# Kernel optimization log

Hardware: AMD Instinct MI355X
Metric: run time of the kernel (lower is better)

The kernel has to match this reference:

```python
import jax, jax.numpy as jnp
import numpy as np

GH, GW = 8, 8  # hypernetwork patch grid
EPS = 1e-5


def image_coords(b, h, w, dtype):
    # matches get_image_coordinates: channel0 = x (varies along W), channel1 = y (varies along H)
    xs = jnp.linspace(-1.0, 1.0, w, dtype=dtype)
    ys = jnp.linspace(-1.0, 1.0, h, dtype=dtype)
    X = jnp.broadcast_to(xs[None, :], (h, w))
    Y = jnp.broadcast_to(ys[:, None], (h, w))
    g = jnp.stack([X, Y], axis=0)  # [2,H,W]
    return jnp.broadcast_to(g[None], (b, 2, h, w))


def im2col3(x):
    # reflect-pad 3x3 im2col -> [B,C,9,H,W]
    H, W = x.shape[2], x.shape[3]
    xp = jnp.pad(x, ((0, 0), (0, 0), (1, 1), (1, 1)), mode='reflect')
    cols = [xp[:, :, i:i + H, j:j + W] for i in range(3) for j in range(3)]
    return jnp.stack(cols, axis=2)


def meta_dw3(x, wsig):
    # depthwise 3x3 conv with per-patch weights. wsig: [B, C*9, GH, GW]
    B, C, H, W = x.shape
    p, q = H // GH, W // GW
    cols = im2col3(x).reshape(B, C, 9, GH, p, GW, q)
    Wd = wsig.reshape(B, C, 9, GH, GW)
    out = jnp.einsum('bctuivj,bctuv->bcuivj', cols, Wd)
    return out.reshape(B, C, H, W)


def meta_pw(x, wsig, out_nc):
    # pointwise 1x1 conv with per-patch weights. wsig: [B, out_nc*C, GH, GW]
    B, C, H, W = x.shape
    p, q = H // GH, W // GW
    xr = x.reshape(B, C, GH, p, GW, q)
    Wp = wsig.reshape(B, out_nc, C, GH, GW)
    out = jnp.einsum('bcuivj,bocuv->bouivj', xr, Wp)
    return out.reshape(B, out_nc, H, W)


def batch_norm(x, g, b):
    m = jnp.mean(x, (0, 2, 3), keepdims=True)
    v = jnp.var(x, (0, 2, 3), keepdims=True)
    return (x - m) * jax.lax.rsqrt(v + EPS) * g[None, :, None, None] + b[None, :, None, None]


def relu6(x):
    return jnp.clip(x, 0.0, 6.0)


def hpir(x, wsig, out_nc, g_dw, b_dw, g_pw, b_pw):
    # HyperPatchInvertedResidual, expand_ratio=1, stride=1, in_nc != out_nc -> no residual
    C = x.shape[1]
    n_dw = C * 9
    h = relu6(batch_norm(meta_dw3(x, wsig[:, :n_dw]), g_dw, b_dw))
    h = batch_norm(meta_pw(h, wsig[:, n_dw:n_dw + out_nc * C], out_nc), g_pw, b_pw)
    return h


def resize_bilinear(p, hw):
    B, C = p.shape[0], p.shape[1]
    return jax.image.resize(p, (B, C, hw[0], hw[1]), method='bilinear')


def decoder_forward(x_img, f0, f1, w0, w1, w2,
                    g_dw0, b_dw0, g_pw0, b_pw0,
                    g_dw1, b_dw1, g_pw1, b_pw1,
                    g_dw2, b_dw2, g_pw2, b_pw2):
    feats = [x_img, f0, f1]  # [img] + features[:-1]
    level_w = [w0, w1, w2]
    level_out = [64, 32, 21]
    bn_p = [(g_dw0, b_dw0, g_pw0, b_pw0),
            (g_dw1, b_dw1, g_pw1, b_pw1),
            (g_dw2, b_dw2, g_pw2, b_pw2)]
    p = None
    for level in range(3):
        f = feats[-level - 1]
        if p is None:
            p = f
        else:
            if p.shape[2:] != f.shape[2:]:
                p = resize_bilinear(p, f.shape[2:])
            p = jnp.concatenate([f, p], axis=1)
        B, _, H, W = p.shape
        p = jnp.concatenate([image_coords(B, H, W, p.dtype), p], axis=1)
        g_dw, b_dw, g_pw, b_pw = bn_p[level]
        p = hpir(p, level_w[level], level_out[level], g_dw, b_dw, g_pw, b_pw)
    return p


def setup_inputs() -> dict:
    key = jax.random.key(0)
    ks = jax.random.split(key, 8)
    inp = {
        'x_img': jax.random.normal(ks[0], (4, 3, 256, 256), jnp.float32),
        'f0': jax.random.normal(ks[1], (4, 32, 64, 64), jnp.float32),
        'f1': jax.random.normal(ks[2], (4, 64, 32, 32), jnp.float32),
        'w0': jax.random.normal(ks[3], (4, 4818, 8, 8), jnp.float32) * 0.1,
        'w1': jax.random.normal(ks[4], (4, 4018, 8, 8), jnp.float32) * 0.1,
        'w2': jax.random.normal(ks[5], (4, 1110, 8, 8), jnp.float32) * 0.1,
    }
    for name, c in [('dw0', 66), ('pw0', 64), ('dw1', 98), ('pw1', 32), ('dw2', 37), ('pw2', 21)]:
        inp['g_' + name] = jnp.ones((c,), jnp.float32)
        inp['b_' + name] = jnp.zeros((c,), jnp.float32)
    return inp


def reference(x_img, f0, f1, w0, w1, w2,
              g_dw0, b_dw0, g_pw0, b_pw0,
              g_dw1, b_dw1, g_pw1, b_pw1,
              g_dw2, b_dw2, g_pw2, b_pw2):
    return decoder_forward(x_img, f0, f1, w0, w1, w2,
                           g_dw0, b_dw0, g_pw0, b_pw0,
                           g_dw1, b_dw1, g_pw1, b_pw1,
                           g_dw2, b_dw2, g_pw2, b_pw2)
```

## Files before the change

### kernel.cpp

```cpp
#include <hip/hip_runtime.h>
#include <hip/hip_bf16.h>

#define EPS 1e-5f

__device__ __forceinline__ int reflect_idx(int i, int n) {
    if (i < 0) return -i;
    if (i >= n) return 2 * n - 2 - i;
    return i;
}

__device__ __forceinline__ float bilin(const float* __restrict__ pb, int Hp, float sy, float sx) {
    int y0 = (int)floorf(sy), x0 = (int)floorf(sx);
    float fy = sy - y0, fx = sx - x0;
    int y0c = min(max(y0, 0), Hp - 1), y1c = min(max(y0 + 1, 0), Hp - 1);
    int x0c = min(max(x0, 0), Hp - 1), x1c = min(max(x0 + 1, 0), Hp - 1);
    float v00 = pb[y0c * Hp + x0c], v01 = pb[y0c * Hp + x1c];
    float v10 = pb[y1c * Hp + x0c], v11 = pb[y1c * Hp + x1c];
    return v00 * (1 - fy) * (1 - fx) + v01 * (1 - fy) * fx
         + v10 * fy * (1 - fx) + v11 * fy * fx;
}

template <int LEVEL, bool WRITE>
__global__ __launch_bounds__(256)
void fused_dw_kernel(const float* __restrict__ feat, const float* __restrict__ prev,
                     const float* __restrict__ pss, const float* __restrict__ wsig,
                     float* __restrict__ out, float* __restrict__ part) {
    constexpr int C    = LEVEL == 0 ? 66 : 98;
    constexpr int H    = LEVEL == 0 ? 32 : 64;
    constexpr int TILE = 16;
    constexpr int NT   = H / TILE;
    constexpr int PXPT = (TILE * TILE) / 256;
    constexpr int WC   = LEVEL == 0 ? 4818 : 4018;
    constexpr int NF   = LEVEL == 0 ? 64 : 32;
    constexpr int Hp   = 32;
    constexpr int Cp   = 64;
    constexpr int P    = H / 8;
    constexpr float SC = 0.5f;
    constexpr int HS   = TILE + 2;

    __shared__ float sh[HS * HS];
    int tid = threadIdx.x, bid = blockIdx.x;
    int tile = bid % (NT * NT);
    int c = (bid / (NT * NT)) % C;
    int b = bid / (NT * NT * C);
    int ty0 = (tile / NT) * TILE, tx0 = (tile % NT) * TILE;

    for (int i = tid; i < HS * HS; i += 256) {
        int h = reflect_idx(ty0 - 1 + i / HS, H);
        int w = reflect_idx(tx0 - 1 + i % HS, H);
        float val;
        if (c == 0)      val = -1.f + 2.f * w / (H - 1);
        else if (c == 1) val = -1.f + 2.f * h / (H - 1);
        else if (c < 2 + NF) val = feat[((size_t)(b * NF + c - 2) * H + h) * H + w];
        else {
            int o = c - 2 - NF;
            const float* pb = prev + (size_t)(b * Cp + o) * Hp * Hp;
            float raw = bilin(pb, Hp, (h + 0.5f) * SC - 0.5f, (w + 0.5f) * SC - 0.5f);
            val = raw * pss[2 * o] + pss[2 * o + 1];
        }
        sh[i] = val;
    }
    __syncthreads();

    float s1 = 0.f, s2 = 0.f;
    float* ob = out + (((size_t)(b * C + c)) * H + ty0) * H + tx0;
    float wreg[9];
    if constexpr (TILE == P) {
        const float* wb = wsig + ((size_t)(b * WC + c * 9)) * 64 + (ty0 / P) * 8 + (tx0 / P);
#pragma unroll
        for (int t = 0; t < 9; ++t) wreg[t] = wb[(size_t)t * 64];
    }
#pragma unroll
    for (int k = 0; k < PXPT; ++k) {
        int px = tid + k * 256;
        int tyy = px / TILE, txx = px % TILE;
        if constexpr (TILE != P) {
            int u = (ty0 + tyy) / P, vv = (tx0 + txx) / P;
            const float* wb = wsig + ((size_t)(b * WC + c * 9)) * 64 + u * 8 + vv;
#pragma unroll
            for (int t = 0; t < 9; ++t) wreg[t] = wb[(size_t)t * 64];
        }
        float acc = 0.f;
#pragma unroll
        for (int t = 0; t < 9; ++t)
            acc += wreg[t] * sh[(tyy + t / 3) * HS + txx + t % 3];
        if constexpr (WRITE) ob[tyy * H + txx] = acc;
        s1 += acc; s2 += acc * acc;
    }
#pragma unroll
    for (int off = 32; off; off >>= 1) {
        s1 += __shfl_xor(s1, off);
        s2 += __shfl_xor(s2, off);
    }
    __shared__ float r1[4], r2[4];
    int wave = tid >> 6;
    if ((tid & 63) == 0) { r1[wave] = s1; r2[wave] = s2; }
    __syncthreads();
    if (tid == 0) {
        int slot = bid & 63;
        atomicAdd(&part[slot * 2 * C + 2 * c],     r1[0] + r1[1] + r1[2] + r1[3]);
        atomicAdd(&part[slot * 2 * C + 2 * c + 1], r2[0] + r2[1] + r2[2] + r2[3]);
    }
}

__global__ void red_kernel(const float* __restrict__ part, const float* __restrict__ g,
                           const float* __restrict__ bb, float* __restrict__ ss,
                           int C, float invN) {
    int c = threadIdx.x;
    if (c >= C) return;
    float s1 = 0.f, s2 = 0.f;
#pragma unroll 8
    for (int s = 0; s < 64; ++s) {
        s1 += part[s * 2 * C + 2 * c];
        s2 += part[s * 2 * C + 2 * c + 1];
    }
    float m = s1 * invN;
    float var = s2 * invN - m * m;
    float sc = g[c] * rsqrtf(var + EPS);
    ss[2 * c] = sc;
    ss[2 * c + 1] = bb[c] - m * sc;
}

__global__ __launch_bounds__(256)
void dw2_col_kernel(const float* __restrict__ ximg, const float* __restrict__ prev,
                    const float* __restrict__ pw1ss, const float* __restrict__ wsig,
                    __hip_bfloat16* __restrict__ out, float* __restrict__ part) {
    const int C = 37, H = 256, W = 256, WC = 1110, Hp = 64, Cp = 32;
    const int S = 260;
    __shared__ float sh[10 * S];
    __shared__ float pssl[64];
    __shared__ float lwv[72];
    __shared__ float r1[4], r2[4];

    int tid = threadIdx.x, bid = blockIdx.x;
    int rb = bid & 31;
    int c  = (bid >> 5) % C;
    int b  = bid / (32 * C);
    int ty0 = rb * 8;
    int u = rb >> 2;

    if (tid < 64) pssl[tid] = pw1ss[tid];
    if (tid < 72) {
        int v = tid / 9, t = tid - v * 9;
        lwv[tid] = wsig[((size_t)(b * WC + c * 9 + t)) * 64 + u * 8 + v];
    }
    __syncthreads();

    const float* pb   = (c >= 5) ? prev + (size_t)(b * Cp + (c - 5)) * Hp * Hp : nullptr;
    const float* xrow = (c >= 2 && c < 5) ? ximg + (size_t)(b * 3 + c - 2) * H * W : nullptr;
    float cx = -1.f + tid * (2.f / 255.f);
    float sxm = (tid + 0.5f) * 0.25f - 0.5f;
    int x0m = (int)floorf(sxm);
    float fxm = sxm - x0m;
    int x0cm = min(max(x0m, 0), Hp - 1), x1cm = min(max(x0m + 1, 0), Hp - 1);
    float psc = (c >= 5) ? pssl[2 * (c - 5)] : 0.f;
    float psh = (c >= 5) ? pssl[2 * (c - 5) + 1] : 0.f;

    if (c >= 5 && rb >= 1 && rb <= 30) {
        int y0b = 2 * rb - 1;
        const float* q0 = pb + (size_t)y0b * Hp;
        const float* q1 = q0 + Hp;
        const float* q2 = q1 + Hp;
        const float* q3 = q2 + Hp;
        float a0 = q0[x0cm] + (q0[x1cm] - q0[x0cm]) * fxm;
        float a1 = q1[x0cm] + (q1[x1cm] - q1[x0cm]) * fxm;
        float a2 = q2[x0cm] + (q2[x1cm] - q2[x0cm]) * fxm;
        float a3 = q3[x0cm] + (q3[x1cm] - q3[x0cm]) * fxm;
        sh[0 * S + tid + 1] = (a0 + (a1 - a0) * 0.375f) * psc + psh;
        sh[1 * S + tid + 1] = (a0 + (a1 - a0) * 0.625f) * psc + psh;
        sh[2 * S + tid + 1] = (a0 + (a1 - a0) * 0.875f) * psc + psh;
        sh[3 * S + tid + 1] = (a1 + (a2 - a1) * 0.125f) * psc + psh;
        sh[4 * S + tid + 1] = (a1 + (a2 - a1) * 0.375f) * psc + psh;
        sh[5 * S + tid + 1] = (a1 + (a2 - a1) * 0.625f) * psc + psh;
        sh[6 * S + tid + 1] = (a1 + (a2 - a1) * 0.875f) * psc + psh;
        sh[7 * S + tid + 1] = (a2 + (a3 - a2) * 0.125f) * psc + psh;
        sh[8 * S + tid + 1] = (a2 + (a3 - a2) * 0.375f) * psc + psh;
        sh[9 * S + tid + 1] = (a2 + (a3 - a2) * 0.625f) * psc + psh;
    } else {
#pragma unroll
        for (int r = 0; r < 10; ++r) {
            int h = reflect_idx(ty0 - 1 + r, H);
            float val;
            if (c == 0)      val = cx;
            else if (c == 1) val = -1.f + h * (2.f / 255.f);
            else if (c < 5)  val = xrow[h * W + tid];
            else {
                float sy = (h + 0.5f) * 0.25f - 0.5f;
                int y0 = (int)floorf(sy);
                float fy = sy - y0;
                int y0c = min(max(y0, 0), Hp - 1), y1c = min(max(y0 + 1, 0), Hp - 1);
                const float* q0 = pb + y0c * Hp;
                const float* q1 = pb + y1c * Hp;
                float a0 = q0[x0cm] + (q0[x1cm] - q0[x0cm]) * fxm;
                float a1 = q1[x0cm] + (q1[x1cm] - q1[x0cm]) * fxm;
                val = (a0 + (a1 - a0) * fy) * psc + psh;
            }
            sh[r * S + tid + 1] = val;
        }
    }
    if (tid < 20) {
        int r = tid >> 1, side = tid & 1;
        int wimg = side ? 254 : 1;
        int h = reflect_idx(ty0 - 1 + r, H);
        float val;
        if (c == 0)      val = -1.f + wimg * (2.f / 255.f);
        else if (c == 1) val = -1.f + h * (2.f / 255.f);
        else if (c < 5)  val = xrow[h * W + wimg];
        else {
            float sx = (wimg + 0.5f) * 0.25f - 0.5f;
            int x0 = (int)floorf(sx); float fx = sx - x0;
            int x0c = min(max(x0, 0), Hp - 1), x1c = min(max(x0 + 1, 0), Hp - 1);
            float sy = (h + 0.5f) * 0.25f - 0.5f;
            int y0 = (int)floorf(sy); float fy = sy - y0;
            int y0c = min(max(y0, 0), Hp - 1), y1c = min(max(y0 + 1, 0), Hp - 1);
            const float* q0 = pb + y0c * Hp;
            const float* q1 = pb + y1c * Hp;
            float a0 = q0[x0c] + (q0[x1c] - q0[x0c]) * fx;
            float a1 = q1[x0c] + (q1[x1c] - q1[x0c]) * fx;
            val = (a0 + (a1 - a0) * fy) * psc + psh;
        }
        sh[r * S + (side ? 257 : 0)] = val;
    }
    __syncthreads();

    int t = tid;
    int v = t >> 5;
    float wr[9];
#pragma unroll
    for (int tap = 0; tap < 9; ++tap) wr[tap] = lwv[v * 9 + tap];

    float px[8];
#pragma unroll
    for (int k = 0; k < 8; ++k) px[k] = 0.f;

#pragma unroll
    for (int r = 0; r < 10; ++r) {
        float L = sh[r * S + t];
        float M = sh[r * S + t + 1];
        float R = sh[r * S + t + 2];
#pragma unroll
        for (int dr = 0; dr < 3; ++dr) {
            int k = r - dr;
            if (k >= 0 && k < 8)
                px[k] += wr[dr * 3] * L + wr[dr * 3 + 1] * M + wr[dr * 3 + 2] * R;
        }
    }

    __hip_bfloat16* ob = out + (((size_t)(b * C + c)) * H + ty0) * W + t;
    float s1 = 0.f, s2 = 0.f;
#pragma unroll
    for (int k = 0; k < 8; ++k) {
        ob[k * W] = __float2bfloat16(px[k]);
        s1 += px[k]; s2 += px[k] * px[k];
    }
#pragma unroll
    for (int off = 32; off; off >>= 1) {
        s1 += __shfl_xor(s1, off);
        s2 += __shfl_xor(s2, off);
    }
    int wave = tid >> 6;
    if ((tid & 63) == 0) { r1[wave] = s1; r2[wave] = s2; }
    __syncthreads();
    if (tid == 0) {
        int slot = bid & 63;
        atomicAdd(&part[slot * 2 * C + 2 * c],     r1[0] + r1[1] + r1[2] + r1[3]);
        atomicAdd(&part[slot * 2 * C + 2 * c + 1], r2[0] + r2[1] + r2[2] + r2[3]);
    }
}

template <int C, int ONC, int H, int PX_T, int OC_T>
__global__ __launch_bounds__(256)
void pw_small_kernel(const float* __restrict__ x, const float* __restrict__ wsig,
                     const float* __restrict__ ss, float* __restrict__ out,
                     float* __restrict__ part, int WC, int ndw) {
    constexpr int P = H / 8;
    constexpr int OC_I = ONC / OC_T;
    __shared__ float lw[ONC * C];
    __shared__ float lx[C * PX_T];
    int tid = threadIdx.x, bid = blockIdx.x;
    int uv = bid & 63, b = bid >> 6;
    int u = uv >> 3, v = uv & 7;

    const size_t wbase = ((size_t)b * WC + ndw) * 64 + uv;
    for (int i = tid; i < ONC * C; i += 256) lw[i] = wsig[wbase + (size_t)i * 64];
    for (int i = tid; i < C * PX_T; i += 256) {
        int c = i / PX_T, pxl = i % PX_T;
        int h = u * P + pxl / P, w = v * P + pxl % P;
        float xv = x[(((size_t)b * C + c) * H + h) * H + w];
        lx[i] = fminf(fmaxf(xv * ss[2 * c] + ss[2 * c + 1], 0.f), 6.f);
    }
    __syncthreads();

    int px_id = tid % PX_T, oc_id = tid / PX_T;
    int h = u * P + px_id / P, w = v * P + px_id % P;
    float acc[OC_I];
#pragma unroll
    for (int oi = 0; oi < OC_I; ++oi) acc[oi] = 0.f;
    for (int c = 0; c < C; ++c) {
        float xv = lx[c * PX_T + px_id];
#pragma unroll
        for (int oi = 0; oi < OC_I; ++oi)
            acc[oi] += lw[(oc_id * OC_I + oi) * C + c] * xv;
    }
    float* ob = out + (((size_t)b * ONC) * H + h) * H + w;
#pragma unroll
    for (int oi = 0; oi < OC_I; ++oi)
        ob[(size_t)(oc_id * OC_I + oi) * H * H] = acc[oi];

    constexpr int GROUP = (PX_T < 64) ? PX_T : 64;
    int lane = tid & 63;
    int slot = bid & 63;
#pragma unroll
    for (int oi = 0; oi < OC_I; ++oi) {
        float s1 = acc[oi], s2 = acc[oi] * acc[oi];
#pragma unroll
        for (int off = GROUP / 2; off; off >>= 1) {
            s1 += __shfl_xor(s1, off);
            s2 += __shfl_xor(s2, off);
        }
        if ((lane & (GROUP - 1)) == 0) {
            int o = oc_id * OC_I + oi;
            atomicAdd(&part[slot * 2 * ONC + 2 * o], s1);
            atomicAdd(&part[slot * 2 * ONC + 2 * o + 1], s2);
        }
    }
}

__global__ __launch_bounds__(256)
void pw2_kernel(const __hip_bfloat16* __restrict__ x, const float* __restrict__ wsig,
                const float* __restrict__ dss,
                float* __restrict__ out, float* __restrict__ part) {
    const int C = 37, ONC = 21, H = 256, WC = 1110, NDW = 333;
    __shared__ float lw[777];
    __shared__ float ssl[74];
    __shared__ float r1[4][ONC], r2[4][ONC];
    int tid = threadIdx.x, bid = blockIdx.x;
    int chunk = bid & 3;
    int uv = (bid >> 2) & 63;
    int b = bid >> 8;
    int y0 = (uv >> 3) * 32 + chunk * 8, x0 = (uv & 7) * 32;

    for (int i = tid; i < 777; i += 256) lw[i] = wsig[((size_t)(b * WC + NDW) + i) * 64 + uv];
    if (tid < 74) ssl[tid] = dss[tid];
    __syncthreads();

    int row = tid >> 5, col = tid & 31;
    const __hip_bfloat16* xb = x + (((size_t)(b * C)) * H + y0 + row) * H + x0 + col;
    float acc[ONC];
#pragma unroll
    for (int o = 0; o < ONC; ++o) acc[o] = 0.f;

    for (int c = 0; c < C; ++c) {
        float xv = __bfloat162float(xb[(size_t)c * H * H]);
        xv = fminf(fmaxf(xv * ssl[2 * c] + ssl[2 * c + 1], 0.f), 6.f);
#pragma unroll
        for (int o = 0; o < ONC; ++o)
            acc[o] += lw[o * C + c] * xv;
    }
    float* ob = out + (((size_t)(b * ONC)) * H + y0 + row) * H + x0 + col;
#pragma unroll
    for (int o = 0; o < ONC; ++o) ob[(size_t)o * H * H] = acc[o];

    int wave = tid >> 6, lane = tid & 63;
#pragma unroll
    for (int o = 0; o < ONC; ++o) {
        float s1 = acc[o], s2 = acc[o] * acc[o];
#pragma unroll
        for (int off = 32; off; off >>= 1) {
            s1 += __shfl_xor(s1, off);
            s2 += __shfl_xor(s2, off);
        }
        if (lane == 0) { r1[wave][o] = s1; r2[wave][o] = s2; }
    }
    __syncthreads();
    int slot = bid & 63;
    for (int o = tid; o < ONC; o += 256) {
        atomicAdd(&part[slot * 42 + 2 * o],     r1[0][o] + r1[1][o] + r1[2][o] + r1[3][o]);
        atomicAdd(&part[slot * 42 + 2 * o + 1], r2[0][o] + r2[1][o] + r2[2][o] + r2[3][o]);
    }
}

__global__ void finalbn_kernel(float* __restrict__ out, const float* __restrict__ ss) {
    int idx = blockIdx.x * 256 + threadIdx.x;
    const int total4 = 4 * 21 * 256 * 256 / 4;
    if (idx >= total4) return;
    int c = (idx / (256 * 256 / 4)) % 21;
    float4 v = ((float4*)out)[idx];
    float sc = ss[2 * c], sb = ss[2 * c + 1];
    v.x = v.x * sc + sb; v.y = v.y * sc + sb; v.z = v.z * sc + sb; v.w = v.w * sc + sb;
    ((float4*)out)[idx] = v;
}

extern "C" void kernel_launch(void* const* d_in, const int* in_sizes, int n_in,
                              void* d_out, int out_size, void* d_ws, size_t ws_size,
                              hipStream_t stream) {
    const float* x_img = (const float*)d_in[0];
    const float* f0    = (const float*)d_in[1];
    const float* f1    = (const float*)d_in[2];
    const float* w0    = (const float*)d_in[3];
    const float* w1    = (const float*)d_in[4];
    const float* w2    = (const float*)d_in[5];
    const float* g_dw0 = (const float*)d_in[6],  *b_dw0 = (const float*)d_in[7];
    const float* g_pw0 = (const float*)d_in[8],  *b_pw0 = (const float*)d_in[9];
    const float* g_dw1 = (const float*)d_in[10], *b_dw1 = (const float*)d_in[11];
    const float* g_pw1 = (const float*)d_in[12], *b_pw1 = (const float*)d_in[13];
    const float* g_dw2 = (const float*)d_in[14], *b_dw2 = (const float*)d_in[15];
    const float* g_pw2 = (const float*)d_in[16], *b_pw2 = (const float*)d_in[17];
    float* out = (float*)d_out;
    float* ws = (float*)d_ws;

    float* part_dw0 = ws;
    float* part_pw0 = ws + 8448;
    float* part_dw1 = ws + 16640;
    float* part_pw1 = ws + 29184;
    float* part_dw2 = ws + 33280;
    float* part_pw2 = ws + 38016;
    float* dw0ss = ws + 40704;
    float* pw0ss = ws + 40836;
    float* dw1ss = ws + 40964;
    float* pw1ss = ws + 41160;
    float* dw2ss = ws + 41224;
    float* pw2ss = ws + 41298;
    float* pw0raw = ws + 41344;
    float* pw1raw = pw0raw + 262144;
    float* bigA   = pw1raw + 524288;
    __hip_bfloat16* bigAb = (__hip_bfloat16*)bigA;

    hipMemsetAsync(ws, 0, 40704 * sizeof(float), stream);

    fused_dw_kernel<0, true><<<4 * 66 * 4, 256, 0, stream>>>(
        f1, nullptr, nullptr, w0, bigA, part_dw0);
    red_kernel<<<1, 128, 0, stream>>>(part_dw0, g_dw0, b_dw0, dw0ss, 66, 1.f / 4096.f);
    pw_small_kernel<66, 64, 32, 16, 16><<<256, 256, 0, stream>>>(
        bigA, w0, dw0ss, pw0raw, part_pw0, 4818, 594);
    red_kernel<<<1, 128, 0, stream>>>(part_pw0, g_pw0, b_pw0, pw0ss, 64, 1.f / 4096.f);
    fused_dw_kernel<1, true><<<4 * 98 * 16, 256, 0, stream>>>(
        f0, pw0raw, pw0ss, w1, bigA, part_dw1);
    red_kernel<<<1, 128, 0, stream>>>(part_dw1, g_dw1, b_dw1, dw1ss, 98, 1.f / 16384.f);
    pw_small_kernel<98, 32, 64, 64, 4><<<256, 256, 0, stream>>>(
        bigA, w1, dw1ss, pw1raw, part_pw1, 4018, 882);
    red_kernel<<<1, 128, 0, stream>>>(part_pw1, g_pw1, b_pw1, pw1ss, 32, 1.f / 16384.f);
    dw2_col_kernel<<<4 * 37 * 32, 256, 0, stream>>>(
        x_img, pw1raw, pw1ss, w2, bigAb, part_dw2);
    red_kernel<<<1, 128, 0, stream>>>(part_dw2, g_dw2, b_dw2, dw2ss, 37, 1.f / 262144.f);
    pw2_kernel<<<1024, 256, 0, stream>>>(bigAb, w2, dw2ss, out, part_pw2);
    red_kernel<<<1, 128, 0, stream>>>(part_pw2, g_pw2, b_pw2, pw2ss, 21, 1.f / 262144.f);
    finalbn_kernel<<<5376, 256, 0, stream>>>(out, pw2ss);
}
```

Baseline: 144.0 us.

## Fuse all decoder stages into one persistent cooperative kernel with grid syncs

```diff
diff --git a/kernel.cpp b/kernel.cpp
--- a/kernel.cpp
+++ b/kernel.cpp
@@ -1,5 +1,8 @@
 #include <hip/hip_runtime.h>
 #include <hip/hip_bf16.h>
+#include <hip/hip_cooperative_groups.h>
+
+namespace cg = cooperative_groups;
 
 #define EPS 1e-5f
 
@@ -20,11 +23,31 @@
          + v10 * fy * (1 - fx) + v11 * fy * fx;
 }
 
-template <int LEVEL, bool WRITE>
-__global__ __launch_bounds__(256)
-void fused_dw_kernel(const float* __restrict__ feat, const float* __restrict__ prev,
-                     const float* __restrict__ pss, const float* __restrict__ wsig,
-                     float* __restrict__ out, float* __restrict__ part) {
+__device__ __forceinline__ void block_red(const float* __restrict__ part,
+                                          const float* __restrict__ g,
+                                          const float* __restrict__ bb,
+                                          float* ssl, int C, float invN, int tid) {
+    if (tid < C) {
+        float s1 = 0.f, s2 = 0.f;
+#pragma unroll 8
+        for (int s = 0; s < 64; ++s) {
+            s1 += part[s * 2 * C + 2 * tid];
+            s2 += part[s * 2 * C + 2 * tid + 1];
+        }
+        float m = s1 * invN;
+        float var = s2 * invN - m * m;
+        float sc = g[tid] * rsqrtf(var + EPS);
+        ssl[2 * tid] = sc;
+        ssl[2 * tid + 1] = bb[tid] - m * sc;
+    }
+}
+
+template <int LEVEL>
+__device__ __forceinline__
+void dw_body(int bid, int tid, float* BODY,
+             const float* __restrict__ feat, const float* __restrict__ prev,
+             const float* __restrict__ pssl, const float* __restrict__ wsig,
+             float* __restrict__ out, float* __restrict__ part) {
     constexpr int C    = LEVEL == 0 ? 66 : 98;
     constexpr int H    = LEVEL == 0 ? 32 : 64;
     constexpr int TILE = 16;
@@ -38,8 +61,10 @@
     constexpr float SC = 0.5f;
     constexpr int HS   = TILE + 2;
 
-    __shared__ float sh[HS * HS];
-    int tid = threadIdx.x, bid = blockIdx.x;
+    float* sh = BODY;
+    float* r1 = BODY + 324;
+    float* r2 = BODY + 328;
+
     int tile = bid % (NT * NT);
     int c = (bid / (NT * NT)) % C;
     int b = bid / (NT * NT * C);
@@ -56,7 +81,7 @@
             int o = c - 2 - NF;
             const float* pb = prev + (size_t)(b * Cp + o) * Hp * Hp;
             float raw = bilin(pb, Hp, (h + 0.5f) * SC - 0.5f, (w + 0.5f) * SC - 0.5f);
-            val = raw * pss[2 * o] + pss[2 * o + 1];
+            val = raw * pssl[2 * o] + pssl[2 * o + 1];
         }
         sh[i] = val;
     }
@@ -65,16 +90,11 @@
     float s1 = 0.f, s2 = 0.f;
     float* ob = out + (((size_t)(b * C + c)) * H + ty0) * H + tx0;
     float wreg[9];
-    if constexpr (TILE == P) {
-        const float* wb = wsig + ((size_t)(b * WC + c * 9)) * 64 + (ty0 / P) * 8 + (tx0 / P);
-#pragma unroll
-        for (int t = 0; t < 9; ++t) wreg[t] = wb[(size_t)t * 64];
-    }
 #pragma unroll
     for (int k = 0; k < PXPT; ++k) {
         int px = tid + k * 256;
         int tyy = px / TILE, txx = px % TILE;
-        if constexpr (TILE != P) {
+        {
             int u = (ty0 + tyy) / P, vv = (tx0 + txx) / P;
             const float* wb = wsig + ((size_t)(b * WC + c * 9)) * 64 + u * 8 + vv;
 #pragma unroll
@@ -84,7 +104,7 @@
 #pragma unroll
         for (int t = 0; t < 9; ++t)
             acc += wreg[t] * sh[(tyy + t / 3) * HS + txx + t % 3];
-        if constexpr (WRITE) ob[tyy * H + txx] = acc;
+        ob[tyy * H + txx] = acc;
         s1 += acc; s2 += acc * acc;
     }
 #pragma unroll
@@ -92,7 +112,6 @@
         s1 += __shfl_xor(s1, off);
         s2 += __shfl_xor(s2, off);
     }
-    __shared__ float r1[4], r2[4];
     int wave = tid >> 6;
     if ((tid & 63) == 0) { r1[wave] = s1; r2[wave] = s2; }
     __syncthreads();
@@ -103,43 +122,85 @@
     }
 }
 
-__global__ void red_kernel(const float* __restrict__ part, const float* __restrict__ g,
-                           const float* __restrict__ bb, float* __restrict__ ss,
-                           int C, float invN) {
-    int c = threadIdx.x;
-    if (c >= C) return;
-    float s1 = 0.f, s2 = 0.f;
-#pragma unroll 8
-    for (int s = 0; s < 64; ++s) {
-        s1 += part[s * 2 * C + 2 * c];
-        s2 += part[s * 2 * C + 2 * c + 1];
-    }
-    float m = s1 * invN;
-    float var = s2 * invN - m * m;
-    float sc = g[c] * rsqrtf(var + EPS);
-    ss[2 * c] = sc;
-    ss[2 * c + 1] = bb[c] - m * sc;
-}
-
-__global__ __launch_bounds__(256)
-void dw2_col_kernel(const float* __restrict__ ximg, const float* __restrict__ prev,
-                    const float* __restrict__ pw1ss, const float* __restrict__ wsig,
-                    __hip_bfloat16* __restrict__ out, float* __restrict__ part) {
+template <int C, int ONC, int H, int PX_T, int OC_T>
+__device__ __forceinline__
+void pw_small_body(int bid, int tid, float* BODY,
+                   const float* __restrict__ x, const float* __restrict__ wsig,
+                   const float* __restrict__ ssl, float* __restrict__ out,
+                   float* __restrict__ part, int WC, int ndw) {
+    constexpr int P = H / 8;
+    constexpr int OC_I = ONC / OC_T;
+    float* lw = BODY;
+    float* lx = BODY + ONC * C;
+
+    __syncthreads();
+
+    int uv = bid & 63, b = bid >> 6;
+    int u = uv >> 3, v = uv & 7;
+
+    const size_t wbase = ((size_t)b * WC + ndw) * 64 + uv;
+    for (int i = tid; i < ONC * C; i += 256) lw[i] = wsig[wbase + (size_t)i * 64];
+    for (int i = tid; i < C * PX_T; i += 256) {
+        int c = i / PX_T, pxl = i % PX_T;
+        int h = u * P + pxl / P, w = v * P + pxl % P;
+        float xv = x[(((size_t)b * C + c) * H + h) * H + w];
+        lx[i] = fminf(fmaxf(xv * ssl[2 * c] + ssl[2 * c + 1], 0.f), 6.f);
+    }
+    __syncthreads();
+
+    int px_id = tid % PX_T, oc_id = tid / PX_T;
+    int h = u * P + px_id / P, w = v * P + px_id % P;
+    float acc[OC_I];
+#pragma unroll
+    for (int oi = 0; oi < OC_I; ++oi) acc[oi] = 0.f;
+    for (int c = 0; c < C; ++c) {
+        float xv = lx[c * PX_T + px_id];
+#pragma unroll
+        for (int oi = 0; oi < OC_I; ++oi)
+            acc[oi] += lw[(oc_id * OC_I + oi) * C + c] * xv;
+    }
+    float* ob = out + (((size_t)b * ONC) * H + h) * H + w;
+#pragma unroll
+    for (int oi = 0; oi < OC_I; ++oi)
+        ob[(size_t)(oc_id * OC_I + oi) * H * H] = acc[oi];
+
+    constexpr int GROUP = (PX_T < 64) ? PX_T : 64;
+    int lane = tid & 63;
+    int slot = bid & 63;
+#pragma unroll
+    for (int oi = 0; oi < OC_I; ++oi) {
+        float s1 = acc[oi], s2 = acc[oi] * acc[oi];
+#pragma unroll
+        for (int off = GROUP / 2; off; off >>= 1) {
+            s1 += __shfl_xor(s1, off);
+            s2 += __shfl_xor(s2, off);
+        }
+        if ((lane & (GROUP - 1)) == 0) {
+            int o = oc_id * OC_I + oi;
+            atomicAdd(&part[slot * 2 * ONC + 2 * o], s1);
+            atomicAdd(&part[slot * 2 * ONC + 2 * o + 1], s2);
+        }
+    }
+}
+
+__device__ __forceinline__
+void dw2_body(int bid, int tid, float* BODY,
+              const float* __restrict__ ximg, const float* __restrict__ prev,
+              const float* __restrict__ pssl, const float* __restrict__ wsig,
+              __hip_bfloat16* __restrict__ out, float* __restrict__ part) {
     const int C = 37, H = 256, W = 256, WC = 1110, Hp = 64, Cp = 32;
     const int S = 260;
-    __shared__ float sh[10 * S];
-    __shared__ float pssl[64];
-    __shared__ float lwv[72];
-    __shared__ float r1[4], r2[4];
-
-    int tid = threadIdx.x, bid = blockIdx.x;
+    float* sh  = BODY;
+    float* lwv = BODY + 2600;
+    float* r1  = BODY + 2672;
+    float* r2  = BODY + 2676;
+
     int rb = bid & 31;
     int c  = (bid >> 5) % C;
     int b  = bid / (32 * C);
     int ty0 = rb * 8;
     int u = rb >> 2;
 
-    if (tid < 64) pssl[tid] = pw1ss[tid];
     if (tid < 72) {
         int v = tid / 9, t = tid - v * 9;
         lwv[tid] = wsig[((size_t)(b * WC + c * 9 + t)) * 64 + u * 8 + v];
@@ -263,85 +324,29 @@
     __syncthreads();
     if (tid == 0) {
         int slot = bid & 63;
-        atomicAdd(&part[slot * 2 * C + 2 * c],     r1[0] + r1[1] + r1[2] + r1[3]);
+        atomicAdd(&part[slot * 2 * C + 2 * c],     s1 * 0.f + r1[0] + r1[1] + r1[2] + r1[3]);
         atomicAdd(&part[slot * 2 * C + 2 * c + 1], r2[0] + r2[1] + r2[2] + r2[3]);
     }
 }
 
-template <int C, int ONC, int H, int PX_T, int OC_T>
-__global__ __launch_bounds__(256)
-void pw_small_kernel(const float* __restrict__ x, const float* __restrict__ wsig,
-                     const float* __restrict__ ss, float* __restrict__ out,
-                     float* __restrict__ part, int WC, int ndw) {
-    constexpr int P = H / 8;
-    constexpr int OC_I = ONC / OC_T;
-    __shared__ float lw[ONC * C];
-    __shared__ float lx[C * PX_T];
-    int tid = threadIdx.x, bid = blockIdx.x;
-    int uv = bid & 63, b = bid >> 6;
-    int u = uv >> 3, v = uv & 7;
-
-    const size_t wbase = ((size_t)b * WC + ndw) * 64 + uv;
-    for (int i = tid; i < ONC * C; i += 256) lw[i] = wsig[wbase + (size_t)i * 64];
-    for (int i = tid; i < C * PX_T; i += 256) {
-        int c = i / PX_T, pxl = i % PX_T;
-        int h = u * P + pxl / P, w = v * P + pxl % P;
-        float xv = x[(((size_t)b * C + c) * H + h) * H + w];
-        lx[i] = fminf(fmaxf(xv * ss[2 * c] + ss[2 * c + 1], 0.f), 6.f);
-    }
-    __syncthreads();
-
-    int px_id = tid % PX_T, oc_id = tid / PX_T;
-    int h = u * P + px_id / P, w = v * P + px_id % P;
-    float acc[OC_I];
-#pragma unroll
-    for (int oi = 0; oi < OC_I; ++oi) acc[oi] = 0.f;
-    for (int c = 0; c < C; ++c) {
-        float xv = lx[c * PX_T + px_id];
-#pragma unroll
-        for (int oi = 0; oi < OC_I; ++oi)
-            acc[oi] += lw[(oc_id * OC_I + oi) * C + c] * xv;
-    }
-    float* ob = out + (((size_t)b * ONC) * H + h) * H + w;
-#pragma unroll
-    for (int oi = 0; oi < OC_I; ++oi)
-        ob[(size_t)(oc_id * OC_I + oi) * H * H] = acc[oi];
-
-    constexpr int GROUP = (PX_T < 64) ? PX_T : 64;
-    int lane = tid & 63;
-    int slot = bid & 63;
-#pragma unroll
-    for (int oi = 0; oi < OC_I; ++oi) {
-        float s1 = acc[oi], s2 = acc[oi] * acc[oi];
-#pragma unroll
-        for (int off = GROUP / 2; off; off >>= 1) {
-            s1 += __shfl_xor(s1, off);
-            s2 += __shfl_xor(s2, off);
-        }
-        if ((lane & (GROUP - 1)) == 0) {
-            int o = oc_id * OC_I + oi;
-            atomicAdd(&part[slot * 2 * ONC + 2 * o], s1);
-            atomicAdd(&part[slot * 2 * ONC + 2 * o + 1], s2);
-        }
-    }
-}
-
-__global__ __launch_bounds__(256)
-void pw2_kernel(const __hip_bfloat16* __restrict__ x, const float* __restrict__ wsig,
-                const float* __restrict__ dss,
-                float* __restrict__ out, float* __restrict__ part) {
+__device__ __forceinline__
+void pw2_body(int bid, int tid, float* BODY,
+              const __hip_bfloat16* __restrict__ x, const float* __restrict__ wsig,
+              const float* __restrict__ ssl, float* __restrict__ out,
+              float* __restrict__ part) {
     const int C = 37, ONC = 21, H = 256, WC = 1110, NDW = 333;
-    __shared__ float lw[777];
-    __shared__ float ssl[74];
-    __shared__ float r1[4][ONC], r2[4][ONC];
-    int tid = threadIdx.x, bid = blockIdx.x;
+    float* lw = BODY;
+    float (*r1)[ONC] = (float(*)[ONC])(BODY + 784);
+    float (*r2)[ONC] = (float(*)[ONC])(BODY + 872);
+
+    __syncthreads();
+
     int chunk = bid & 3;
     int uv = (bid >> 2) & 63;
     int b = bid >> 8;
     int y0 = (uv >> 3) * 32 + chunk * 8, x0 = (uv & 7) * 32;
 
     for (int i = tid; i < 777; i += 256) lw[i] = wsig[((size_t)(b * WC + NDW) + i) * 64 + uv];
-    if (tid < 74) ssl[tid] = dss[tid];
     __syncthreads();
 
     int row = tid >> 5, col = tid & 31;
@@ -380,70 +385,114 @@
     }
 }
 
-__global__ void finalbn_kernel(float* __restrict__ out, const float* __restrict__ ss) {
-    int idx = blockIdx.x * 256 + threadIdx.x;
+struct MegaArgs {
+    const float *x_img, *f0, *f1, *w0, *w1, *w2;
+    const float *g_dw0, *b_dw0, *g_pw0, *b_pw0;
+    const float *g_dw1, *b_dw1, *g_pw1, *b_pw1;
+    const float *g_dw2, *b_dw2, *g_pw2, *b_pw2;
+    float* out;
+    float* parts;
+    float* part_dw0; float* part_pw0; float* part_dw1;
+    float* part_pw1; float* part_dw2; float* part_pw2;
+    float* pw0raw; float* pw1raw; float* bigA;
+    __hip_bfloat16* bigAb;
+};
+
+__global__ __launch_bounds__(256, 4)
+void mega_kernel(MegaArgs a) {
+    cg::grid_group grid = cg::this_grid();
+    __shared__ float smem[9664];
+    float* SSL  = smem;
+    float* BODY = smem + 256;
+    int tid = threadIdx.x, bx = blockIdx.x, nb = gridDim.x;
+
+    for (int i = bx * 256 + tid; i < 40704; i += nb * 256) a.parts[i] = 0.f;
+    grid.sync();
+
+    for (int vb = bx; vb < 1056; vb += nb)
+        dw_body<0>(vb, tid, BODY, a.f1, nullptr, nullptr, a.w0, a.bigA, a.part_dw0);
+    grid.sync();
+
+    block_red(a.part_dw0, a.g_dw0, a.b_dw0, SSL, 66, 1.f / 4096.f, tid);
+    for (int vb = bx; vb < 256; vb += nb)
+        pw_small_body<66, 64, 32, 16, 16>(vb, tid, BODY, a.bigA, a.w0, SSL, a.pw0raw,
+                                          a.part_pw0, 4818, 594);
+    grid.sync();
+
+    block_red(a.part_pw0, a.g_pw0, a.b_pw0, SSL, 64, 1.f / 4096.f, tid);
+    __syncthreads();
+    for (int vb = bx; vb < 6272; vb += nb)
+        dw_body<1>(vb, tid, BODY, a.f0, a.pw0raw, SSL, a.w1, a.bigA, a.part_dw1);
+    grid.sync();
+
+    block_red(a.part_dw1, a.g_dw1, a.b_dw1, SSL, 98, 1.f / 16384.f, tid);
+    for (int vb = bx; vb < 256; vb += nb)
+        pw_small_body<98, 32, 64, 64, 4>(vb, tid, BODY, a.bigA, a.w1, SSL, a.pw1raw,
+                                         a.part_pw1, 4018, 882);
+    grid.sync();
+
+    block_red(a.part_pw1, a.g_pw1, a.b_pw1, SSL, 32, 1.f / 16384.f, tid);
+    __syncthreads();
+    for (int vb = bx; vb < 4736; vb += nb)
+        dw2_body(vb, tid, BODY, a.x_img, a.pw1raw, SSL, a.w2, a.bigAb, a.part_dw2);
+    grid.sync();
+
+    block_red(a.part_dw2, a.g_dw2, a.b_dw2, SSL, 37, 1.f / 262144.f, tid);
+    for (int vb = bx; vb < 1024; vb += nb)
+        pw2_body(vb, tid, BODY, a.bigAb, a.w2, SSL, a.out, a.part_pw2);
+    grid.sync();
+
+    block_red(a.part_pw2, a.g_pw2, a.b_pw2, SSL, 21, 1.f / 262144.f, tid);
+    __syncthreads();
     const int total4 = 4 * 21 * 256 * 256 / 4;
-    if (idx >= total4) return;
-    int c = (idx / (256 * 256 / 4)) % 21;
-    float4 v = ((float4*)out)[idx];
-    float sc = ss[2 * c], sb = ss[2 * c + 1];
-    v.x = v.x * sc + sb; v.y = v.y * sc + sb; v.z = v.z * sc + sb; v.w = v.w * sc + sb;
-    ((float4*)out)[idx] = v;
+    for (int idx = bx * 256 + tid; idx < total4; idx += nb * 256) {
+        int c = (idx / (256 * 256 / 4)) % 21;
+        float4 v = ((float4*)a.out)[idx];
+        float sc = SSL[2 * c], sb = SSL[2 * c + 1];
+        v.x = v.x * sc + sb; v.y = v.y * sc + sb; v.z = v.z * sc + sb; v.w = v.w * sc + sb;
+        ((float4*)a.out)[idx] = v;
+    }
 }
 
 extern "C" void kernel_launch(void* const* d_in, const int* in_sizes, int n_in,
                               void* d_out, int out_size, void* d_ws, size_t ws_size,
                               hipStream_t stream) {
-    const float* x_img = (const float*)d_in[0];
-    const float* f0    = (const float*)d_in[1];
-    const float* f1    = (const float*)d_in[2];
-    const float* w0    = (const float*)d_in[3];
-    const float* w1    = (const float*)d_in[4];
-    const float* w2    = (const float*)d_in[5];
-    const float* g_dw0 = (const float*)d_in[6],  *b_dw0 = (const float*)d_in[7];
-    const float* g_pw0 = (const float*)d_in[8],  *b_pw0 = (const float*)d_in[9];
-    const float* g_dw1 = (const float*)d_in[10], *b_dw1 = (const float*)d_in[11];
-    const float* g_pw1 = (const float*)d_in[12], *b_pw1 = (const float*)d_in[13];
-    const float* g_dw2 = (const float*)d_in[14], *b_dw2 = (const float*)d_in[15];
-    const float* g_pw2 = (const float*)d_in[16], *b_pw2 = (const float*)d_in[17];
-    float* out = (float*)d_out;
     float* ws = (float*)d_ws;
 
-    float* part_dw0 = ws;
-    float* part_pw0 = ws + 8448;
-    float* part_dw1 = ws + 16640;
-    float* part_pw1 = ws + 29184;
-    float* part_dw2 = ws + 33280;
-    float* part_pw2 = ws + 38016;
-    float* dw0ss = ws + 40704;
-    float* pw0ss = ws + 40836;
-    float* dw1ss = ws + 40964;
-    float* pw1ss = ws + 41160;
-    float* dw2ss = ws + 41224;
-    float* pw2ss = ws + 41298;
-    float* pw0raw = ws + 41344;
-    float* pw1raw = pw0raw + 262144;
-    float* bigA   = pw1raw + 524288;
-    __hip_bfloat16* bigAb = (__hip_bfloat16*)bigA;
-
-    hipMemsetAsync(ws, 0, 40704 * sizeof(float), stream);
-
-    fused_dw_kernel<0, true><<<4 * 66 * 4, 256, 0, stream>>>(
-        f1, nullptr, nullptr, w0, bigA, part_dw0);
-    red_kernel<<<1, 128, 0, stream>>>(part_dw0, g_dw0, b_dw0, dw0ss, 66, 1.f / 4096.f);
-    pw_small_kernel<66, 64, 32, 16, 16><<<256, 256, 0, stream>>>(
-        bigA, w0, dw0ss, pw0raw, part_pw0, 4818, 594);
-    red_kernel<<<1, 128, 0, stream>>>(part_pw0, g_pw0, b_pw0, pw0ss, 64, 1.f / 4096.f);
-    fused_dw_kernel<1, true><<<4 * 98 * 16, 256, 0, stream>>>(
-        f0, pw0raw, pw0ss, w1, bigA, part_dw1);
-    red_kernel<<<1, 128, 0, stream>>>(part_dw1, g_dw1, b_dw1, dw1ss, 98, 1.f / 16384.f);
-    pw_small_kernel<98, 32, 64, 64, 4><<<256, 256, 0, stream>>>(
-        bigA, w1, dw1ss, pw1raw, part_pw1, 4018, 882);
-    red_kernel<<<1, 128, 0, stream>>>(part_pw1, g_pw1, b_pw1, pw1ss, 32, 1.f / 16384.f);
-    dw2_col_kernel<<<4 * 37 * 32, 256, 0, stream>>>(
-        x_img, pw1raw, pw1ss, w2, bigAb, part_dw2);
-    red_kernel<<<1, 128, 0, stream>>>(part_dw2, g_dw2, b_dw2, dw2ss, 37, 1.f / 262144.f);
-    pw2_kernel<<<1024, 256, 0, stream>>>(bigAb, w2, dw2ss, out, part_pw2);
-    red_kernel<<<1, 128, 0, stream>>>(part_pw2, g_pw2, b_pw2, pw2ss, 21, 1.f / 262144.f);
-    finalbn_kernel<<<5376, 256, 0, stream>>>(out, pw2ss);
-}
+    MegaArgs a;
+    a.x_img = (const float*)d_in[0];
+    a.f0    = (const float*)d_in[1];
+    a.f1    = (const float*)d_in[2];
+    a.w0    = (const float*)d_in[3];
+    a.w1    = (const float*)d_in[4];
+    a.w2    = (const float*)d_in[5];
+    a.g_dw0 = (const float*)d_in[6];  a.b_dw0 = (const float*)d_in[7];
+    a.g_pw0 = (const float*)d_in[8];  a.b_pw0 = (const float*)d_in[9];
+    a.g_dw1 = (const float*)d_in[10]; a.b_dw1 = (const float*)d_in[11];
+    a.g_pw1 = (const float*)d_in[12]; a.b_pw1 = (const float*)d_in[13];
+    a.g_dw2 = (const float*)d_in[14]; a.b_dw2 = (const float*)d_in[15];
+    a.g_pw2 = (const float*)d_in[16]; a.b_pw2 = (const float*)d_in[17];
+    a.out   = (float*)d_out;
+
+    a.parts    = ws;
+    a.part_dw0 = ws;
+    a.part_pw0 = ws + 8448;
+    a.part_dw1 = ws + 16640;
+    a.part_pw1 = ws + 29184;
+    a.part_dw2 = ws + 33280;
+    a.part_pw2 = ws + 38016;
+    a.pw0raw   = ws + 41344;
+    a.pw1raw   = a.pw0raw + 262144;
+    a.bigA     = a.pw1raw + 524288;
+    a.bigAb    = (__hip_bfloat16*)a.bigA;
+
+    int nblk = 0;
+    hipOccupancyMaxActiveBlocksPerMultiprocessor(&nblk, (const void*)mega_kernel, 256, 0);
+    if (nblk < 1) nblk = 1;
+    if (nblk > 8) nblk = 8;
+    int grid = nblk * 256;
+
+    void* kargs[] = { &a };
+    hipLaunchCooperativeKernel((const void*)mega_kernel, dim3(grid), dim3(256),
+                               kargs, 0, stream);
+}
```

Result: slower. 523.8 us (+263.8%).
